# Optimization experiments

Hardware: AMD Instinct MI355X
Metric: run time of the kernel (lower is better)

## Reference

```python
import jax, jax.numpy as jnp
import numpy as np

TEMPERATURE = 0.05
EPS = 1e-8  # torch.cosine_similarity eps


def setup_inputs() -> dict:
    key = jax.random.key(0)
    k1, k2 = jax.random.split(key)
    N, D = 8192, 256
    text_embeddings = jax.random.normal(k1, (N, D), dtype=jnp.float32)
    text_pos_embeddings = jax.random.normal(k2, (N, D), dtype=jnp.float32)
    return {"text_embeddings": text_embeddings, "text_pos_embeddings": text_pos_embeddings}


def reference(text_embeddings, text_pos_embeddings):
    # cosine similarity via normalize + single GEMM (same math as broadcasted
    # torch.cosine_similarity, which clamps norms at eps)
    a_norm = jnp.maximum(jnp.linalg.norm(text_embeddings, axis=-1, keepdims=True), EPS)
    b_norm = jnp.maximum(jnp.linalg.norm(text_pos_embeddings, axis=-1, keepdims=True), EPS)
    a = text_embeddings / a_norm  # [N, D]
    b = text_pos_embeddings / b_norm  # [N, D]
    sim = jnp.einsum("nd,md->nm", a, b) / TEMPERATURE  # [N, N]
    # cross-entropy with labels = arange(N): mean over rows of -log_softmax diag
    logp = jax.nn.log_softmax(sim, axis=-1)
    loss = -jnp.mean(jnp.diagonal(logp))
    return loss
```

## Files before the change

### kernel.cpp

```cpp
#include <hip/hip_runtime.h>
#include <math.h>

#define DIM 256

typedef float f32x4 __attribute__((ext_vector_type(4)));
typedef int   i32x8 __attribute__((ext_vector_type(8)));

__constant__ const float kTempInvLog2e = 20.0f * 1.4426950408889634f;
#define LN2 0.6931471805599453f
#define EPS_NORM 1e-8f
#define SCALE_ONE 0x7F7F7F7Fu

static __device__ inline unsigned f2fp8x4(float4 v, float s) {
    int r = 0;
    r = __builtin_amdgcn_cvt_pk_fp8_f32(v.x * s, v.y * s, r, false);
    r = __builtin_amdgcn_cvt_pk_fp8_f32(v.z * s, v.w * s, r, true);
    return (unsigned)r;
}

static __device__ inline i32x8 ld_frag32(const void* p0, const void* p1) {
    uint4 a = *(const uint4*)p0;
    uint4 b = *(const uint4*)p1;
    i32x8 v;
    v[0] = a.x; v[1] = a.y; v[2] = a.z; v[3] = a.w;
    v[4] = b.x; v[5] = b.y; v[6] = b.z; v[7] = b.w;
    return v;
}

__global__ __launch_bounds__(256) void normpack_kernel(
    const float* __restrict__ A, const float* __restrict__ B,
    unsigned char* __restrict__ Apk, unsigned char* __restrict__ Bpk,
    float* __restrict__ diag, float* __restrict__ rowsum, int n)
{
    __shared__ uint4 lA[256];
    __shared__ uint4 lB[256];
    const int t = threadIdx.x;
    const int rl = t >> 4;
    const int c16 = t & 15;
    const int r = blockIdx.x * 16 + rl;

    const float4* pa = (const float4*)(A + (size_t)r * DIM + c16 * 16);
    const float4* pb = (const float4*)(B + (size_t)r * DIM + c16 * 16);
    float4 a0 = pa[0], a1 = pa[1], a2 = pa[2], a3 = pa[3];
    float4 b0 = pb[0], b1 = pb[1], b2 = pb[2], b3 = pb[3];

    float ssa = a0.x*a0.x + a0.y*a0.y + a0.z*a0.z + a0.w*a0.w
              + a1.x*a1.x + a1.y*a1.y + a1.z*a1.z + a1.w*a1.w
              + a2.x*a2.x + a2.y*a2.y + a2.z*a2.z + a2.w*a2.w
              + a3.x*a3.x + a3.y*a3.y + a3.z*a3.z + a3.w*a3.w;
    float ssb = b0.x*b0.x + b0.y*b0.y + b0.z*b0.z + b0.w*b0.w
              + b1.x*b1.x + b1.y*b1.y + b1.z*b1.z + b1.w*b1.w
              + b2.x*b2.x + b2.y*b2.y + b2.z*b2.z + b2.w*b2.w
              + b3.x*b3.x + b3.y*b3.y + b3.z*b3.z + b3.w*b3.w;
    float dd  = a0.x*b0.x + a0.y*b0.y + a0.z*b0.z + a0.w*b0.w
              + a1.x*b1.x + a1.y*b1.y + a1.z*b1.z + a1.w*b1.w
              + a2.x*b2.x + a2.y*b2.y + a2.z*b2.z + a2.w*b2.w
              + a3.x*b3.x + a3.y*b3.y + a3.z*b3.z + a3.w*b3.w;
#pragma unroll
    for (int m = 1; m < 16; m <<= 1) {
        ssa += __shfl_xor(ssa, m, 64);
        ssb += __shfl_xor(ssb, m, 64);
        dd  += __shfl_xor(dd, m, 64);
    }
    float na = fmaxf(sqrtf(ssa), EPS_NORM);
    float nb = fmaxf(sqrtf(ssb), EPS_NORM);
    float sa = kTempInvLog2e / na;
    float sb = 1.0f / nb;
    if (c16 == 0) {
        diag[r] = dd / (na * nb) * kTempInvLog2e;
        rowsum[r] = 0.0f;
    }

    const int u = ((c16 >> 3) << 7) + ((c16 & 1) << 6) + rl + ((c16 & 7) >> 1) * 16;
    uint4 ga, gb;
    ga.x = f2fp8x4(a0, sa); ga.y = f2fp8x4(a1, sa);
    ga.z = f2fp8x4(a2, sa); ga.w = f2fp8x4(a3, sa);
    gb.x = f2fp8x4(b0, sb); gb.y = f2fp8x4(b1, sb);
    gb.z = f2fp8x4(b2, sb); gb.w = f2fp8x4(b3, sb);
    lA[u] = ga; lB[u] = gb;
    __syncthreads();

    ((uint4*)Apk)[(size_t)blockIdx.x * 256 + t] = lA[t];
    ((uint4*)Bpk)[(size_t)blockIdx.x * 256 + t] = lB[t];
}

static __device__ inline void async_copy16(const void* g, void* l) {
    __builtin_amdgcn_global_load_lds(
        (const __attribute__((address_space(1))) unsigned int*)g,
        (__attribute__((address_space(3))) unsigned int*)l, 16, 0, 0);
}

__global__ __launch_bounds__(256, 2) void gemm_lse_kernel(
    const unsigned char* __restrict__ Apk, const unsigned char* __restrict__ Bpk,
    float* __restrict__ rowsum, int n)
{
    __shared__ char ldsbuf[16384];
    const int lane = threadIdx.x & 63;
    const int w = threadIdx.x >> 6;
    const int c = lane & 15;
    const int q = lane >> 4;

    const int i = blockIdx.x;
    const int split = ((i & 7) << 1) | ((i >> 3) & 1);
    const int rowblk = i >> 4;
    const int rowbase = rowblk * 256 + w * 64;

    i32x8 afrag[4][2];
#pragma unroll
    for (int m = 0; m < 4; ++m) {
        const int AT = rowblk * 16 + w * 4 + m;
#pragma unroll
        for (int kc = 0; kc < 2; ++kc) {
            const char* base = (const char*)Apk + ((size_t)AT * 2 + kc) * 2048 + lane * 16;
            afrag[m][kc] = ld_frag32(base, base + 1024);
        }
    }

    float sums[16];
#pragma unroll
    for (int s = 0; s < 16; ++s) sums[s] = 0.0f;

    const char* bbase = (const char*)Bpk + (size_t)split * 32 * 4096;
    const int niter = 16;

    {
        const char* src = bbase + w * 2048 + (size_t)lane * 16;
        char* dst = ldsbuf + w * 2048;
        async_copy16(src, dst);
        async_copy16(src + 1024, dst + 1024);
    }
    __syncthreads();

    for (int it = 0; it < niter; ++it) {
#pragma unroll
        for (int m = 0; m < 4; ++m)
#pragma unroll
            for (int kc = 0; kc < 2; ++kc)
                asm volatile("" : "+v"(afrag[m][kc]));

        const int cur = it & 1;
        if (it + 1 < niter) {
            const char* src = bbase + (size_t)(it + 1) * 8192 + w * 2048 + (size_t)lane * 16;
            char* dst = ldsbuf + (cur ^ 1) * 8192 + w * 2048;
            async_copy16(src, dst);
            async_copy16(src + 1024, dst + 1024);
        }

        f32x4 acc[4][2];
#pragma unroll
        for (int m = 0; m < 4; ++m)
#pragma unroll
            for (int nc = 0; nc < 2; ++nc)
                acc[m][nc] = (f32x4){0.f, 0.f, 0.f, 0.f};

        const char* lb = ldsbuf + cur * 8192 + (size_t)lane * 16;
#pragma unroll
        for (int nc = 0; nc < 2; ++nc) {
#pragma unroll
            for (int kc = 0; kc < 2; ++kc) {
                const char* p = lb + nc * 4096 + kc * 2048;
                i32x8 bfrag = ld_frag32(p, p + 1024);
#pragma unroll
                for (int m = 0; m < 4; ++m)
                    acc[m][nc] = __builtin_amdgcn_mfma_scale_f32_16x16x128_f8f6f4(
                        afrag[m][kc], bfrag, acc[m][nc],
                        0, 0,
                        0, SCALE_ONE,
                        0, SCALE_ONE);
            }
        }

#pragma unroll
        for (int m = 0; m < 4; ++m)
#pragma unroll
            for (int nc = 0; nc < 2; ++nc)
#pragma unroll
                for (int r = 0; r < 4; ++r)
                    sums[m * 4 + r] += __builtin_amdgcn_exp2f(acc[m][nc][r]);

        __syncthreads();
    }

#pragma unroll
    for (int s = 0; s < 16; ++s) {
        float v = sums[s];
        v += __shfl_xor(v, 1, 64);
        v += __shfl_xor(v, 2, 64);
        v += __shfl_xor(v, 4, 64);
        v += __shfl_xor(v, 8, 64);
        sums[s] = v;
    }
    if (c == 0) {
#pragma unroll
        for (int m = 0; m < 4; ++m)
#pragma unroll
            for (int r = 0; r < 4; ++r)
                atomicAdd(&rowsum[rowbase + m * 16 + q * 4 + r], sums[m * 4 + r]);
    }
}

__global__ __launch_bounds__(1024) void finale_kernel(
    const float* __restrict__ rowsum, const float* __restrict__ diag,
    float* __restrict__ out, int n)
{
    __shared__ float red[1024];
    float local = 0.0f;
    for (int row = threadIdx.x; row < n; row += 1024)
        local += log2f(rowsum[row]) - diag[row];
    red[threadIdx.x] = local;
    __syncthreads();
    for (int off = 512; off > 0; off >>= 1) {
        if (threadIdx.x < off) red[threadIdx.x] += red[threadIdx.x + off];
        __syncthreads();
    }
    if (threadIdx.x == 0) out[0] = red[0] * (LN2 / (float)n);
}

extern "C" void kernel_launch(void* const* d_in, const int* in_sizes, int n_in,
                              void* d_out, int out_size, void* d_ws, size_t ws_size,
                              hipStream_t stream) {
    const int n = in_sizes[0] / DIM;
    const float* A = (const float*)d_in[0];
    const float* B = (const float*)d_in[1];
    float* out = (float*)d_out;

    unsigned char* Apk = (unsigned char*)d_ws;
    unsigned char* Bpk = Apk + (size_t)n * DIM;
    float* rowsum = (float*)(Bpk + (size_t)n * DIM);
    float* diag = rowsum + n;

    normpack_kernel<<<n / 16, 256, 0, stream>>>(A, B, Apk, Bpk, diag, rowsum, n);

    gemm_lse_kernel<<<(n / 256) * 16, 256, 0, stream>>>(Apk, Bpk, rowsum, n);

    finale_kernel<<<1, 1024, 0, stream>>>(rowsum, diag, out, n);
}
```

Baseline: 89.40 us.

## Software-pipeline MFMA and exp2 stages across ping-pong accumulator sets

Unrolls the GEMM loop by two and keeps two accumulator sets, so the exp2 reduction of one tile's results is issued after the MFMAs of the next tile. The aim is to overlap transcendental VALU work with matrix-core execution instead of serialising them within each iteration. This costs extra accumulator registers (32 more VGPRs), which may pressure the two-blocks-per-CU launch bound.

```diff
diff --git a/kernel.cpp b/kernel.cpp
--- a/kernel.cpp
+++ b/kernel.cpp
@@ -121,7 +121,6 @@
     for (int s = 0; s < 16; ++s) sums[s] = 0.0f;
 
     const char* bbase = (const char*)Bpk + (size_t)split * 32 * 4096;
-    const int niter = 16;
 
     {
         const char* src = bbase + w * 2048 + (size_t)lane * 16;
@@ -131,55 +130,57 @@
     }
     __syncthreads();
 
-    for (int it = 0; it < niter; ++it) {
-#pragma unroll
-        for (int m = 0; m < 4; ++m)
-#pragma unroll
-            for (int kc = 0; kc < 2; ++kc)
-                asm volatile("" : "+v"(afrag[m][kc]));
-
-        const int cur = it & 1;
-        if (it + 1 < niter) {
-            const char* src = bbase + (size_t)(it + 1) * 8192 + w * 2048 + (size_t)lane * 16;
-            char* dst = ldsbuf + (cur ^ 1) * 8192 + w * 2048;
-            async_copy16(src, dst);
-            async_copy16(src + 1024, dst + 1024);
-        }
-
-        f32x4 acc[4][2];
-#pragma unroll
-        for (int m = 0; m < 4; ++m)
-#pragma unroll
-            for (int nc = 0; nc < 2; ++nc)
-                acc[m][nc] = (f32x4){0.f, 0.f, 0.f, 0.f};
-
-        const char* lb = ldsbuf + cur * 8192 + (size_t)lane * 16;
-#pragma unroll
-        for (int nc = 0; nc < 2; ++nc) {
-#pragma unroll
-            for (int kc = 0; kc < 2; ++kc) {
-                const char* p = lb + nc * 4096 + kc * 2048;
-                i32x8 bfrag = ld_frag32(p, p + 1024);
-#pragma unroll
-                for (int m = 0; m < 4; ++m)
-                    acc[m][nc] = __builtin_amdgcn_mfma_scale_f32_16x16x128_f8f6f4(
-                        afrag[m][kc], bfrag, acc[m][nc],
-                        0, 0,
-                        0, SCALE_ONE,
-                        0, SCALE_ONE);
-            }
-        }
-
-#pragma unroll
-        for (int m = 0; m < 4; ++m)
-#pragma unroll
-            for (int nc = 0; nc < 2; ++nc)
-#pragma unroll
-                for (int r = 0; r < 4; ++r)
-                    sums[m * 4 + r] += __builtin_amdgcn_exp2f(acc[m][nc][r]);
-
+    f32x4 accA[4][2], accB[4][2];
+
+#define PREFETCH(IT, BUF) do {                                               \
+    const char* _src = bbase + (size_t)(IT) * 8192 + w * 2048 + (size_t)lane * 16; \
+    char* _dst = ldsbuf + (BUF) * 8192 + w * 2048;                           \
+    async_copy16(_src, _dst);                                                \
+    async_copy16(_src + 1024, _dst + 1024);                                  \
+} while (0)
+
+#define MFMA_TILE(ACC, BUF) do {                                             \
+    _Pragma("unroll") for (int m = 0; m < 4; ++m)                            \
+        _Pragma("unroll") for (int kc = 0; kc < 2; ++kc)                     \
+            asm volatile("" : "+v"(afrag[m][kc]));        \
+    const char* _lb = ldsbuf + (BUF) * 8192 + (size_t)lane * 16;             \
+    _Pragma("unroll") for (int m = 0; m < 4; ++m)                            \
+        _Pragma("unroll") for (int nc = 0; nc < 2; ++nc)                     \
+            ACC[m][nc] = (f32x4){0.f, 0.f, 0.f, 0.f};                        \
+    _Pragma("unroll") for (int nc = 0; nc < 2; ++nc)                         \
+        _Pragma("unroll") for (int kc = 0; kc < 2; ++kc) {                   \
+            const char* _p = _lb + nc * 4096 + kc * 2048;                    \
+            i32x8 _bf = ld_frag32(_p, _p + 1024);                            \
+            _Pragma("unroll") for (int m = 0; m < 4; ++m)                    \
+                ACC[m][nc] = __builtin_amdgcn_mfma_scale_f32_16x16x128_f8f6f4( \
+                    afrag[m][kc], _bf, ACC[m][nc],                           \
+                    0, 0, 0, SCALE_ONE, 0, SCALE_ONE);                       \
+        }                                                                    \
+} while (0)
+
+#define EXP_TILE(ACC) do {                                                   \
+    _Pragma("unroll") for (int m = 0; m < 4; ++m)                            \
+        _Pragma("unroll") for (int nc = 0; nc < 2; ++nc)                     \
+            _Pragma("unroll") for (int r = 0; r < 4; ++r)                    \
+                sums[m * 4 + r] += __builtin_amdgcn_exp2f(ACC[m][nc][r]);    \
+} while (0)
+
+#pragma unroll 1
+    for (int itp = 0; itp < 8; ++itp) {
+        PREFETCH(2 * itp + 1, 1);
+        MFMA_TILE(accA, 0);
+        if (itp > 0) EXP_TILE(accB);
         __syncthreads();
-    }
+        if (itp < 7) PREFETCH(2 * itp + 2, 0);
+        MFMA_TILE(accB, 1);
+        EXP_TILE(accA);
+        __syncthreads();
+    }
+    EXP_TILE(accB);
+
+#undef PREFETCH
+#undef MFMA_TILE
+#undef EXP_TILE
 
 #pragma unroll
     for (int s = 0; s < 16; ++s) {
```

Result: no change. 90.99 us (+1.8%).
